# Performance work log

Measured on AMD Instinct MI355X. Metric: run time of the kernel, lower is better.

## Reference

```python
import jax, jax.numpy as jnp
import numpy as np

TEMPERATURE = 0.5


def setup_inputs() -> dict:
    key = jax.random.key(0)
    k1, k2 = jax.random.split(key)
    N, Z = 4096, 2048
    z1 = jax.random.normal(k1, (N, Z), dtype=jnp.float32)
    z2 = jax.random.normal(k2, (N, Z), dtype=jnp.float32)
    return {"z1": z1, "z2": z2}


def reference(z1, z2):
    # NT-Xent loss. Original torch code: normalize, build full 2Nx2N cosine-sim
    # matrix, prepend the positive pair column, cross-entropy with label 0.
    # Mathematically, per-row CE with the positive prepended and the self-sim
    # removed equals: logsumexp over the row excluding the diagonal, minus the
    # positive logit.  (cosine_similarity on already-normalized vectors is a
    # plain dot product, so normalization is applied once.)
    n, _ = z1.shape
    a = z1 / jnp.linalg.norm(z1, axis=1, keepdims=True)  # [N, Z]
    b = z2 / jnp.linalg.norm(z2, axis=1, keepdims=True)  # [N, Z]
    reps = jnp.concatenate([a, b], axis=0)               # [2N, Z]
    logits = jnp.matmul(reps, reps.T) / TEMPERATURE      # [2N, 2N]
    NEG_INF = jnp.float32(-1e9)  # mask self-similarity (excluded from CE denom)
    logits = jnp.where(jnp.eye(2 * n, dtype=bool), NEG_INF, logits)
    pos = jnp.sum(a * b, axis=1) / TEMPERATURE           # [N] positive logits
    pos = jnp.concatenate([pos, pos])                    # [2N]
    lse = jax.nn.logsumexp(logits, axis=1)               # [2N]
    # sum of CE over 2N rows, divided by 2N  == mean
    return jnp.mean(lse - pos)
```

## Files before the change

### kernel.cpp

```cpp
#include <hip/hip_runtime.h>
#include <stdint.h>

#define N_ROWS 4096
#define Z_DIM  2048
#define TOT    8192
#define TILE   128
#define RBYTES (Z_DIM / 2)
#define BKE    128
#define KBYT   (BKE / 2)
#define NITER  (Z_DIM / BKE)
#define NT     (TOT / TILE)
#define NBLK   (NT * (NT + 1) / 2)
#define INV_T  2.0f
#define SCL4   64.0f

typedef __attribute__((ext_vector_type(4))) int   intx4;
typedef __attribute__((ext_vector_type(8))) int   intx8;
typedef __attribute__((ext_vector_type(4))) float floatx4;

#define GLOAD16(g, l)                                                   \
    __builtin_amdgcn_global_load_lds(                                   \
        (const __attribute__((address_space(1))) unsigned int*)(g),     \
        (__attribute__((address_space(3))) unsigned int*)(l), 16, 0, 0)

__device__ __forceinline__ unsigned int f2fp4(float v) {
    float a = fabsf(v);
    unsigned int c = (a >= 0.25f) + (a >= 0.75f) + (a >= 1.25f) + (a >= 1.75f)
                   + (a >= 2.5f)  + (a >= 3.5f)  + (a >= 5.0f);
    return c | (v < 0.f ? 8u : 0u);
}

__global__ __launch_bounds__(256) void normalize_kernel(
    const float* __restrict__ z1, const float* __restrict__ z2,
    unsigned char* __restrict__ reps, float* __restrict__ pos,
    float* __restrict__ rowsum)
{
    const int row  = blockIdx.x;
    const int tid  = threadIdx.x;
    const int lane = tid & 63, wave = tid >> 6;

    if (row < TOT / 256) rowsum[row * 256 + tid] = 0.f;

    const float4* p1 = (const float4*)(z1 + (size_t)row * Z_DIM);
    const float4* p2 = (const float4*)(z2 + (size_t)row * Z_DIM);
    float4 x0 = p1[tid * 2], x1 = p1[tid * 2 + 1];
    float4 y0 = p2[tid * 2], y1 = p2[tid * 2 + 1];

    float s1 = x0.x*x0.x + x0.y*x0.y + x0.z*x0.z + x0.w*x0.w
             + x1.x*x1.x + x1.y*x1.y + x1.z*x1.z + x1.w*x1.w;
    float s2 = y0.x*y0.x + y0.y*y0.y + y0.z*y0.z + y0.w*y0.w
             + y1.x*y1.x + y1.y*y1.y + y1.z*y1.z + y1.w*y1.w;
    float dd = x0.x*y0.x + x0.y*y0.y + x0.z*y0.z + x0.w*y0.w
             + x1.x*y1.x + x1.y*y1.y + x1.z*y1.z + x1.w*y1.w;

    #pragma unroll
    for (int m = 1; m < 64; m <<= 1) {
        s1 += __shfl_xor(s1, m);
        s2 += __shfl_xor(s2, m);
        dd += __shfl_xor(dd, m);
    }
    __shared__ float red[3][4];
    if (lane == 0) { red[0][wave] = s1; red[1][wave] = s2; red[2][wave] = dd; }
    __syncthreads();
    s1 = red[0][0] + red[0][1] + red[0][2] + red[0][3];
    s2 = red[1][0] + red[1][1] + red[1][2] + red[1][3];
    dd = red[2][0] + red[2][1] + red[2][2] + red[2][3];

    const float inv1 = rsqrtf(s1), inv2 = rsqrtf(s2);
    if (tid == 0) {
        float p = dd * inv1 * inv2 * INV_T;
        pos[row] = p;
        pos[row + N_ROWS] = p;
    }

    const float a = inv1 * SCL4, b = inv2 * SCL4;
    unsigned int pa =  f2fp4(x0.x * a)        | (f2fp4(x0.y * a) << 4)
                    | (f2fp4(x0.z * a) << 8)  | (f2fp4(x0.w * a) << 12)
                    | (f2fp4(x1.x * a) << 16) | (f2fp4(x1.y * a) << 20)
                    | (f2fp4(x1.z * a) << 24) | (f2fp4(x1.w * a) << 28);
    unsigned int pb =  f2fp4(y0.x * b)        | (f2fp4(y0.y * b) << 4)
                    | (f2fp4(y0.z * b) << 8)  | (f2fp4(y0.w * b) << 12)
                    | (f2fp4(y1.x * b) << 16) | (f2fp4(y1.y * b) << 20)
                    | (f2fp4(y1.z * b) << 24) | (f2fp4(y1.w * b) << 28);
    *(unsigned int*)(reps + (size_t)row * RBYTES + tid * 4) = pa;
    *(unsigned int*)(reps + (size_t)(N_ROWS + row) * RBYTES + tid * 4) = pb;
}

__global__ __launch_bounds__(256) void simclr_gemm(
    const unsigned char* __restrict__ reps, float* __restrict__ rowsum)
{
    __shared__ __align__(16) unsigned char L[2][2][TILE * KBYT];

    const int t = blockIdx.x;
    int r = (int)((sqrtf(8.0f * (float)t + 1.0f) - 1.0f) * 0.5f);
    while ((r + 1) * (r + 2) / 2 <= t) ++r;
    while (r * (r + 1) / 2 > t) --r;
    const int bi = t - r * (r + 1) / 2;
    const int bj = r;
    const bool diag = (bi == bj);

    const int tid  = threadIdx.x;
    const int lane = tid & 63, wave = tid >> 6;
    const int wr = wave >> 1, wc = wave & 1;
    const int quad = lane >> 4, l16 = lane & 15;
    const int sw   = (l16 >> 1) & 3;
    const int row0 = bi * TILE, col0 = bj * TILE;

    floatx4 acc[4][4];
    #pragma unroll
    for (int i = 0; i < 4; ++i)
        #pragma unroll
        for (int j = 0; j < 4; ++j)
            acc[i][j] = floatx4{0.f, 0.f, 0.f, 0.f};

    const int c0 = tid, c1 = tid + 256;
    const int r0s = c0 >> 2, k0s = (c0 & 3) ^ ((r0s >> 1) & 3);
    const int r1s = c1 >> 2, k1s = (c1 & 3) ^ ((r1s >> 1) & 3);
    const unsigned char* gA0 = reps + (size_t)(row0 + r0s) * RBYTES + k0s * 16;
    const unsigned char* gA1 = reps + (size_t)(row0 + r1s) * RBYTES + k1s * 16;
    const unsigned char* gB0 = reps + (size_t)(col0 + r0s) * RBYTES + k0s * 16;
    const unsigned char* gB1 = reps + (size_t)(col0 + r1s) * RBYTES + k1s * 16;
    const int o0 = c0 * 16, o1 = c1 * 16;

    GLOAD16(gA0, &L[0][0][o0]);
    GLOAD16(gA1, &L[0][0][o1]);
    GLOAD16(gB0, &L[0][1][o0]);
    GLOAD16(gB1, &L[0][1][o1]);
    __syncthreads();

    for (int i = 0; i < NITER; ++i) {
        if (i + 1 < NITER) {
            const size_t ko = (size_t)(i + 1) * KBYT;
            const int buf = (i + 1) & 1;
            GLOAD16(gA0 + ko, &L[buf][0][o0]);
            GLOAD16(gA1 + ko, &L[buf][0][o1]);
            GLOAD16(gB0 + ko, &L[buf][1][o0]);
            GLOAD16(gB1 + ko, &L[buf][1][o1]);
        }
        const unsigned char* Ab = &L[i & 1][0][0];
        const unsigned char* Bb = &L[i & 1][1][0];

        intx8 af[4], bf[4];
        #pragma unroll
        for (int fi = 0; fi < 4; ++fi) {
            const int ar = (wr * 64 + fi * 16 + l16) * KBYT;
            const int br = (wc * 64 + fi * 16 + l16) * KBYT;
            intx4 av = *(const intx4*)&Ab[ar + ((quad ^ sw) << 4)];
            intx4 bv = *(const intx4*)&Bb[br + ((quad ^ sw) << 4)];
            af[fi] = intx8{av[0], av[1], av[2], av[3], 0, 0, 0, 0};
            bf[fi] = intx8{bv[0], bv[1], bv[2], bv[3], 0, 0, 0, 0};
        }
        #pragma unroll
        for (int fi = 0; fi < 4; ++fi)
            #pragma unroll
            for (int j = 0; j < 4; ++j)
                acc[fi][j] = __builtin_amdgcn_mfma_scale_f32_16x16x128_f8f6f4(
                    af[fi], bf[j], acc[fi][j],
                    4, 4,
                    0, 0x7F7F7F7Fu,
                    0, 0x7F7F7F7Fu);
        __syncthreads();
    }

    const float descale = INV_T / (SCL4 * SCL4);
    float scol[4] = {0.f, 0.f, 0.f, 0.f};
    #pragma unroll
    for (int fi = 0; fi < 4; ++fi) {
        const int rbase = row0 + wr * 64 + fi * 16 + quad * 4;
        float srow[4] = {0.f, 0.f, 0.f, 0.f};
        #pragma unroll
        for (int j = 0; j < 4; ++j) {
            const int c = col0 + wc * 64 + j * 16 + l16;
            #pragma unroll
            for (int rr = 0; rr < 4; ++rr) {
                float e = __expf(acc[fi][j][rr] * descale);
                if (diag && (rbase + rr == c)) e = 0.f;
                srow[rr] += e;
                scol[j]  += e;
            }
        }
        #pragma unroll
        for (int rr = 0; rr < 4; ++rr) {
            #pragma unroll
            for (int m = 1; m < 16; m <<= 1) srow[rr] += __shfl_xor(srow[rr], m);
        }
        if (l16 == 0) {
            #pragma unroll
            for (int rr = 0; rr < 4; ++rr)
                atomicAdd(&rowsum[rbase + rr], srow[rr]);
        }
    }
    if (!diag) {
        #pragma unroll
        for (int j = 0; j < 4; ++j) {
            scol[j] += __shfl_xor(scol[j], 16);
            scol[j] += __shfl_xor(scol[j], 32);
        }
        if (quad == 0) {
            #pragma unroll
            for (int j = 0; j < 4; ++j)
                atomicAdd(&rowsum[col0 + wc * 64 + j * 16 + l16], scol[j]);
        }
    }
}

__global__ __launch_bounds__(1024) void finalize_kernel(
    const float* __restrict__ rowsum, const float* __restrict__ pos,
    float* __restrict__ out)
{
    const int tid = threadIdx.x;
    const int lane = tid & 63, wave = tid >> 6;
    float s = 0.f;
    for (int r = tid; r < TOT; r += 1024) s += logf(rowsum[r]) - pos[r];
    #pragma unroll
    for (int m = 1; m < 64; m <<= 1) s += __shfl_xor(s, m);
    __shared__ float red[16];
    if (lane == 0) red[wave] = s;
    __syncthreads();
    if (tid == 0) {
        float t = 0.f;
        #pragma unroll
        for (int w = 0; w < 16; ++w) t += red[w];
        out[0] = t * (1.0f / TOT);
    }
}

extern "C" void kernel_launch(void* const* d_in, const int* in_sizes, int n_in,
                              void* d_out, int out_size, void* d_ws, size_t ws_size,
                              hipStream_t stream)
{
    const float* z1 = (const float*)d_in[0];
    const float* z2 = (const float*)d_in[1];
    float* out = (float*)d_out;

    char* w = (char*)d_ws;
    unsigned char* reps = (unsigned char*)w;
    float* pos    = (float*)(w + (size_t)TOT * RBYTES);
    float* rowsum = pos + TOT;

    normalize_kernel<<<N_ROWS, 256, 0, stream>>>(z1, z2, reps, pos, rowsum);
    simclr_gemm<<<NBLK, 256, 0, stream>>>(reps, rowsum);
    finalize_kernel<<<1, 1024, 0, stream>>>(rowsum, pos, out);
}
```

Baseline: 156.8 us.

## Triple-buffer LDS with vmcnt waits, setprio on MFMA, and XCD-aware block remap

Moves the GEMM K-loop from double to triple-buffered LDS. It prefetches two stages ahead and uses explicit s_waitcnt vmcnt plus a single barrier per iteration in place of __syncthreads, so global loads overlap more with compute. It also raises wave priority around the MFMA block and remaps blockIdx so consecutive tiles land on the same XCD for better L2 locality. This costs extra LDS per block, which may reduce occupancy, and relies on hand-counted outstanding loads. The remap assumes NBLK is divisible by 8 (NBLK=2080, which it is).

```diff
diff --git a/kernel.cpp b/kernel.cpp
--- a/kernel.cpp
+++ b/kernel.cpp
@@ -89,9 +89,10 @@
 __global__ __launch_bounds__(256) void simclr_gemm(
     const unsigned char* __restrict__ reps, float* __restrict__ rowsum)
 {
-    __shared__ __align__(16) unsigned char L[2][2][TILE * KBYT];
-
-    const int t = blockIdx.x;
+    __shared__ __align__(16) unsigned char L[3][2][TILE * KBYT];
+
+    const int bid = blockIdx.x;
+    const int t = (bid & 7) * (NBLK / 8) + (bid >> 3);
     int r = (int)((sqrtf(8.0f * (float)t + 1.0f) - 1.0f) * 0.5f);
     while ((r + 1) * (r + 2) / 2 <= t) ++r;
     while (r * (r + 1) / 2 > t) --r;
@@ -126,19 +127,29 @@
     GLOAD16(gA1, &L[0][0][o1]);
     GLOAD16(gB0, &L[0][1][o0]);
     GLOAD16(gB1, &L[0][1][o1]);
-    __syncthreads();
-
+    GLOAD16(gA0 + KBYT, &L[1][0][o0]);
+    GLOAD16(gA1 + KBYT, &L[1][0][o1]);
+    GLOAD16(gB0 + KBYT, &L[1][1][o0]);
+    GLOAD16(gB1 + KBYT, &L[1][1][o1]);
+
+    int cur = 0;
+    #pragma unroll 1
     for (int i = 0; i < NITER; ++i) {
-        if (i + 1 < NITER) {
-            const size_t ko = (size_t)(i + 1) * KBYT;
-            const int buf = (i + 1) & 1;
-            GLOAD16(gA0 + ko, &L[buf][0][o0]);
-            GLOAD16(gA1 + ko, &L[buf][0][o1]);
-            GLOAD16(gB0 + ko, &L[buf][1][o0]);
-            GLOAD16(gB1 + ko, &L[buf][1][o1]);
-        }
-        const unsigned char* Ab = &L[i & 1][0][0];
-        const unsigned char* Bb = &L[i & 1][1][0];
+        if (i + 1 < NITER) asm volatile("s_waitcnt vmcnt(4)" ::: "memory");
+        else               asm volatile("s_waitcnt vmcnt(0)" ::: "memory");
+        __builtin_amdgcn_s_barrier();
+        asm volatile("" ::: "memory");
+
+        if (i + 2 < NITER) {
+            const size_t ko = (size_t)(i + 2) * KBYT;
+            int pf = cur + 2; if (pf >= 3) pf -= 3;
+            GLOAD16(gA0 + ko, &L[pf][0][o0]);
+            GLOAD16(gA1 + ko, &L[pf][0][o1]);
+            GLOAD16(gB0 + ko, &L[pf][1][o0]);
+            GLOAD16(gB1 + ko, &L[pf][1][o1]);
+        }
+        const unsigned char* Ab = &L[cur][0][0];
+        const unsigned char* Bb = &L[cur][1][0];
 
         intx8 af[4], bf[4];
         #pragma unroll
@@ -150,6 +161,7 @@
             af[fi] = intx8{av[0], av[1], av[2], av[3], 0, 0, 0, 0};
             bf[fi] = intx8{bv[0], bv[1], bv[2], bv[3], 0, 0, 0, 0};
         }
+        __builtin_amdgcn_s_setprio(1);
         #pragma unroll
         for (int fi = 0; fi < 4; ++fi)
             #pragma unroll
@@ -159,7 +171,8 @@
                     4, 4,
                     0, 0x7F7F7F7Fu,
                     0, 0x7F7F7F7Fu);
-        __syncthreads();
+        __builtin_amdgcn_s_setprio(0);
+        cur = (cur == 2) ? 0 : cur + 1;
     }
 
     const float descale = INV_T / (SCL4 * SCL4);
```

After: 149.1 us. 4.9% less time.

## Load MFMA fragments directly from global into registers, drop LDS staging

Applied to the files above, without the earlier changes.

Removes the LDS double buffer and per-iteration __syncthreads: each lane now loads its A/B fp4 fragments straight from global memory into registers, prefetching the next K slice into a second register set. It also remaps block IDs with a stride-8 interleave to spread triangular tiles across XCDs, and raises wave priority around the MFMA block. Each wave now reads its own fragments, so tile data is no longer shared through LDS within a workgroup and more global/L2 traffic results. Loads of 16 bytes per lane from rows 1 KB apart are also poorly coalesced.

```diff
diff --git a/kernel.cpp b/kernel.cpp
--- a/kernel.cpp
+++ b/kernel.cpp
@@ -18,11 +18,6 @@
 typedef __attribute__((ext_vector_type(8))) int   intx8;
 typedef __attribute__((ext_vector_type(4))) float floatx4;
 
-#define GLOAD16(g, l)                                                   \
-    __builtin_amdgcn_global_load_lds(                                   \
-        (const __attribute__((address_space(1))) unsigned int*)(g),     \
-        (__attribute__((address_space(3))) unsigned int*)(l), 16, 0, 0)
-
 __device__ __forceinline__ unsigned int f2fp4(float v) {
     float a = fabsf(v);
     unsigned int c = (a >= 0.25f) + (a >= 0.75f) + (a >= 1.25f) + (a >= 1.75f)
@@ -89,9 +84,8 @@
 __global__ __launch_bounds__(256) void simclr_gemm(
     const unsigned char* __restrict__ reps, float* __restrict__ rowsum)
 {
-    __shared__ __align__(16) unsigned char L[2][2][TILE * KBYT];
-
-    const int t = blockIdx.x;
+    const int bid = blockIdx.x;
+    const int t = (bid & 7) * (NBLK / 8) + (bid >> 3);
     int r = (int)((sqrtf(8.0f * (float)t + 1.0f) - 1.0f) * 0.5f);
     while ((r + 1) * (r + 2) / 2 <= t) ++r;
     while (r * (r + 1) / 2 > t) --r;
@@ -103,7 +97,6 @@
     const int lane = tid & 63, wave = tid >> 6;
     const int wr = wave >> 1, wc = wave & 1;
     const int quad = lane >> 4, l16 = lane & 15;
-    const int sw   = (l16 >> 1) & 3;
     const int row0 = bi * TILE, col0 = bj * TILE;
 
     floatx4 acc[4][4];
@@ -113,43 +106,42 @@
         for (int j = 0; j < 4; ++j)
             acc[i][j] = floatx4{0.f, 0.f, 0.f, 0.f};
 
-    const int c0 = tid, c1 = tid + 256;
-    const int r0s = c0 >> 2, k0s = (c0 & 3) ^ ((r0s >> 1) & 3);
-    const int r1s = c1 >> 2, k1s = (c1 & 3) ^ ((r1s >> 1) & 3);
-    const unsigned char* gA0 = reps + (size_t)(row0 + r0s) * RBYTES + k0s * 16;
-    const unsigned char* gA1 = reps + (size_t)(row0 + r1s) * RBYTES + k1s * 16;
-    const unsigned char* gB0 = reps + (size_t)(col0 + r0s) * RBYTES + k0s * 16;
-    const unsigned char* gB1 = reps + (size_t)(col0 + r1s) * RBYTES + k1s * 16;
-    const int o0 = c0 * 16, o1 = c1 * 16;
-
-    GLOAD16(gA0, &L[0][0][o0]);
-    GLOAD16(gA1, &L[0][0][o1]);
-    GLOAD16(gB0, &L[0][1][o0]);
-    GLOAD16(gB1, &L[0][1][o1]);
-    __syncthreads();
-
+    const unsigned char* pA[4];
+    const unsigned char* pB[4];
+    #pragma unroll
+    for (int fi = 0; fi < 4; ++fi) {
+        pA[fi] = reps + (size_t)(row0 + wr * 64 + fi * 16 + l16) * RBYTES
+                      + quad * 16;
+        pB[fi] = reps + (size_t)(col0 + wc * 64 + fi * 16 + l16) * RBYTES
+                      + quad * 16;
+    }
+
+    intx4 ca[4], cb[4];
+    #pragma unroll
+    for (int fi = 0; fi < 4; ++fi) {
+        ca[fi] = *(const intx4*)pA[fi];
+        cb[fi] = *(const intx4*)pB[fi];
+    }
+
+    #pragma unroll 2
     for (int i = 0; i < NITER; ++i) {
+        intx4 na[4], nb[4];
         if (i + 1 < NITER) {
-            const size_t ko = (size_t)(i + 1) * KBYT;
-            const int buf = (i + 1) & 1;
-            GLOAD16(gA0 + ko, &L[buf][0][o0]);
-            GLOAD16(gA1 + ko, &L[buf][0][o1]);
-            GLOAD16(gB0 + ko, &L[buf][1][o0]);
-            GLOAD16(gB1 + ko, &L[buf][1][o1]);
-        }
-        const unsigned char* Ab = &L[i & 1][0][0];
-        const unsigned char* Bb = &L[i & 1][1][0];
+            const int ko = (i + 1) * KBYT;
+            #pragma unroll
+            for (int fi = 0; fi < 4; ++fi) {
+                na[fi] = *(const intx4*)(pA[fi] + ko);
+                nb[fi] = *(const intx4*)(pB[fi] + ko);
+            }
+        }
 
         intx8 af[4], bf[4];
         #pragma unroll
         for (int fi = 0; fi < 4; ++fi) {
-            const int ar = (wr * 64 + fi * 16 + l16) * KBYT;
-            const int br = (wc * 64 + fi * 16 + l16) * KBYT;
-            intx4 av = *(const intx4*)&Ab[ar + ((quad ^ sw) << 4)];
-            intx4 bv = *(const intx4*)&Bb[br + ((quad ^ sw) << 4)];
-            af[fi] = intx8{av[0], av[1], av[2], av[3], 0, 0, 0, 0};
-            bf[fi] = intx8{bv[0], bv[1], bv[2], bv[3], 0, 0, 0, 0};
-        }
+            af[fi] = intx8{ca[fi][0], ca[fi][1], ca[fi][2], ca[fi][3], 0,0,0,0};
+            bf[fi] = intx8{cb[fi][0], cb[fi][1], cb[fi][2], cb[fi][3], 0,0,0,0};
+        }
+        __builtin_amdgcn_s_setprio(1);
         #pragma unroll
         for (int fi = 0; fi < 4; ++fi)
             #pragma unroll
@@ -159,7 +151,12 @@
                     4, 4,
                     0, 0x7F7F7F7Fu,
                     0, 0x7F7F7F7Fu);
-        __syncthreads();
+        __builtin_amdgcn_s_setprio(0);
+
+        if (i + 1 < NITER) {
+            #pragma unroll
+            for (int fi = 0; fi < 4; ++fi) { ca[fi] = na[fi]; cb[fi] = nb[fi]; }
+        }
     }
 
     const float descale = INV_T / (SCL4 * SCL4);
```

Result: slower. 228.7 us (+45.9%).
